# Kernel optimization log

Measured on AMD Instinct MI355X. Metric: run time of the kernel, lower is better.

Reference implementation:

```python
import jax, jax.numpy as jnp
import numpy as np

N = 200_000      # active voxels
C_IN = 128
C_OUT = 128
GRID = 128
K = 27           # 3x3x3 submanifold kernel offsets
EPS = 1e-4       # scn BatchNormalization default eps
LEAK = 0.333     # scn LeakyReLU default leakiness


def _build_neighbor_idx(rng):
    # unique active voxel coords via unique linear keys in GRID^3
    keys = rng.choice(GRID ** 3, size=N, replace=False).astype(np.int64)
    z = keys % GRID
    y = (keys // GRID) % GRID
    x = keys // (GRID * GRID)
    coords = np.stack([x, y, z], axis=1)  # [N,3]
    order = np.argsort(keys)
    sorted_keys = keys[order]
    offs = np.array([(dx, dy, dz) for dx in (-1, 0, 1)
                     for dy in (-1, 0, 1) for dz in (-1, 0, 1)], dtype=np.int64)
    nb = np.full((N, K), -1, dtype=np.int32)
    for k in range(K):
        q = coords + offs[k]  # [N,3]
        inb = np.all((q >= 0) & (q < GRID), axis=1)
        qk = (q[:, 0] * GRID + q[:, 1]) * GRID + q[:, 2]
        pos = np.searchsorted(sorted_keys, qk)
        pos = np.clip(pos, 0, N - 1)
        hit = inb & (sorted_keys[pos] == qk)
        nb[:, k] = np.where(hit, order[pos].astype(np.int32), -1)
    return nb


def setup_inputs() -> dict:
    key = jax.random.key(0)
    k1, k2 = jax.random.split(key)
    rng = np.random.default_rng(0)
    neighbor_idx = jnp.asarray(_build_neighbor_idx(rng))       # [N,27] int32, -1 = inactive
    features = jax.random.normal(k1, (N, C_IN), dtype=jnp.float32)
    # per-offset conv weights, scn-style init scale
    W = jax.random.normal(k2, (K, C_IN, C_OUT), dtype=jnp.float32) * (1.0 / np.sqrt(K * C_IN))
    b = jnp.zeros((C_OUT,), dtype=jnp.float32)
    gamma = jnp.ones((C_OUT,), dtype=jnp.float32)
    beta = jnp.zeros((C_OUT,), dtype=jnp.float32)
    return {"features": features, "W": W, "b": b, "gamma": gamma,
            "beta": beta, "neighbor_idx": neighbor_idx}


def reference(features, W, b, gamma, beta, neighbor_idx):
    # Submanifold 3D conv: output only at active sites; gather active neighbors.
    valid = (neighbor_idx >= 0)                      # [N,27] bool
    idx = jnp.where(valid, neighbor_idx, 0)          # safe gather index
    out = jnp.broadcast_to(b, (features.shape[0], C_OUT))
    for k in range(K):  # fixed structural loop over 27 kernel offsets
        xk = features[idx[:, k]] * valid[:, k:k + 1].astype(features.dtype)  # [N,C_IN]
        out = out + xk @ W[k]                                                # [N,C_OUT]
    # BatchNormalization over all active sites (training-mode batch stats)
    mean = jnp.mean(out, axis=0)
    var = jnp.var(out, axis=0)
    out = (out - mean) * jax.lax.rsqrt(var + EPS) * gamma + beta
    # LeakyReLU (scn default leakiness 0.333)
    return jnp.where(out > 0, out, LEAK * out)
```

## Files before the change

kernel.cpp:

```cpp
#include <hip/hip_runtime.h>
#include <hip/hip_bf16.h>

#define N_VOX 200000
#define CI 128
#define CO 128
#define KK 27
#define BM 128
#define NBLK 1563
#define NSTEP 54
#define LEAK 0.333f
#define BN_EPS 1e-4f

typedef unsigned short u16;
typedef unsigned int u32;
typedef __attribute__((ext_vector_type(8))) short short8;
typedef __attribute__((ext_vector_type(4))) float f32x4;

typedef const __attribute__((address_space(1))) u32* gptr_t;
typedef __attribute__((address_space(3))) u32* lptr_t;

__device__ __forceinline__ u16 f2bf(float f) {
  union { float f; u32 u; } x; x.f = f;
  return (u16)((x.u + 0x7FFFu + ((x.u >> 16) & 1u)) >> 16);
}
__device__ __forceinline__ u16 cvt_bf(float f) {
  union { __hip_bfloat16 h; u16 u; } c;
  c.h = __float2bfloat16(f);
  return c.u;
}

__global__ __launch_bounds__(256) void wcast_kernel(const float* __restrict__ W,
                                                    u16* __restrict__ Wt) {
  __shared__ float tile[32][33];
  int k = blockIdx.z;
  int ci0 = blockIdx.y * 32, co0 = blockIdx.x * 32;
  const float* Wk = W + (size_t)k * CI * CO;
  u16* Wtk = Wt + (size_t)k * CI * CO;
  int tx = threadIdx.x, ty = threadIdx.y;
#pragma unroll
  for (int j = 0; j < 4; ++j)
    tile[ty + j * 8][tx] = Wk[(ci0 + ty + j * 8) * CO + co0 + tx];
  __syncthreads();
#pragma unroll
  for (int j = 0; j < 4; ++j) {
    int co = co0 + ty + j * 8;
    int ci = ci0 + tx;
    Wtk[co * CI + (ci ^ ((co & 7) << 3))] = f2bf(tile[tx][ty + j * 8]);
  }
}

__global__ __launch_bounds__(256, 2) void conv_kernel(
    const float* __restrict__ feat, const u16* __restrict__ Wt,
    const int* __restrict__ nb, float* __restrict__ out,
    float* __restrict__ partial) {
  __shared__ __align__(16) char smem[79360];
  u16* const Ab0 = (u16*)smem;
  u16* const Ab1 = (u16*)(smem + 16384);
  u16* const Bb0 = (u16*)(smem + 32768);
  u16* const Bb1 = (u16*)(smem + 49152);
  int* const nbs = (int*)(smem + 65536);
  float* const sq = (float*)(smem + 65536);

  const int tid = threadIdx.x;
  const int bid = blockIdx.x;
  const int row0 = bid * BM;

  for (int i = tid; i < BM * KK; i += 256) {
    int gi = row0 * KK + i;
    nbs[i] = (gi < N_VOX * KK) ? nb[gi] : -1;
  }
  __syncthreads();

  const int lane = tid & 63;
  const int wv = tid >> 6;
  const int wr = wv >> 1, wc = wv & 1;
  const int lr = lane & 15, lg = lane >> 4;
  const int arow = tid >> 1;
  const int acol = (tid & 1) * 32;

  f32x4 acc[4][4];
#pragma unroll
  for (int m = 0; m < 4; ++m)
#pragma unroll
    for (int n = 0; n < 4; ++n) acc[m][n] = (f32x4){0.f, 0.f, 0.f, 0.f};

  float4 af[8];

  auto issueA = [&](int s) {
    int k = s >> 1, half = (s & 1) * 64;
    int src = nbs[arow * KK + k];
    if (src >= 0) {
      const float4* p = (const float4*)(feat + (size_t)src * CI + half + acol);
#pragma unroll
      for (int j = 0; j < 8; ++j) af[j] = p[j];
    } else {
#pragma unroll
      for (int j = 0; j < 8; ++j) af[j] = (float4){0.f, 0.f, 0.f, 0.f};
    }
  };

  auto issueB = [&](int s, u16* Bdst) {
    int k = s >> 1, half = (s & 1) * 64;
    const u16* base = Wt + (size_t)k * CO * CI + half;
#pragma unroll
    for (int j = 0; j < 4; ++j) {
      int cbase = (tid >> 6) * 64 + 256 * j;
      int c = cbase + (tid & 63);
      int co = c >> 3, sub = c & 7;
      gptr_t g = (gptr_t)(base + (size_t)co * CI + sub * 8);
      __builtin_amdgcn_global_load_lds(g, (lptr_t)(Bdst + cbase * 8), 16, 0, 0);
    }
  };

  auto writeA = [&](u16* Adst) {
    int v = arow & 7;
#pragma unroll
    for (int q = 0; q < 4; ++q) {
      u16 t8[8];
#pragma unroll
      for (int i = 0; i < 2; ++i) {
        float4 f = af[q * 2 + i];
        t8[i * 4 + 0] = cvt_bf(f.x); t8[i * 4 + 1] = cvt_bf(f.y);
        t8[i * 4 + 2] = cvt_bf(f.z); t8[i * 4 + 3] = cvt_bf(f.w);
      }
      int c_o = (tid & 1) * 4 + q;
      *(uint4*)&Adst[arow * 64 + ((c_o ^ v) << 3)] = *(const uint4*)t8;
    }
  };

  auto compute = [&](const u16* A, const u16* B) {
#pragma unroll
    for (int ks = 0; ks < 2; ++ks) {
      short8 a[4], b[4];
#pragma unroll
      for (int m = 0; m < 4; ++m) {
        int r = wr * 64 + m * 16 + lr;
        a[m] = *(const short8*)((const char*)(A + r * 64) +
                                ((ks * 64 + lg * 16) ^ ((r & 7) << 4)));
      }
#pragma unroll
      for (int n = 0; n < 4; ++n) {
        int cn = wc * 64 + n * 16 + lr;
        b[n] = *(const short8*)((const char*)(B + cn * 64) +
                                ((ks * 64 + lg * 16) ^ ((cn & 7) << 4)));
      }
#pragma unroll
      for (int m = 0; m < 4; ++m)
#pragma unroll
        for (int n = 0; n < 4; ++n)
          acc[m][n] = __builtin_amdgcn_mfma_f32_16x16x32_bf16(a[m], b[n], acc[m][n], 0, 0, 0);
    }
  };

  issueA(0);
  issueB(0, Bb0);
  for (int s = 0; s < NSTEP - 1; ++s) {
    int pb = s & 1;
    u16* Ac = pb ? Ab1 : Ab0;
    u16* Bc = pb ? Bb1 : Bb0;
    u16* Bn = pb ? Bb0 : Bb1;
    writeA(Ac);
    __syncthreads();
    issueA(s + 1);
    issueB(s + 1, Bn);
    compute(Ac, Bc);
  }
  writeA(Ab1);
  __syncthreads();
  compute(Ab1, Bb1);

  float sv[4], qv[4];
#pragma unroll
  for (int n = 0; n < 4; ++n) {
    float s = 0.f, q = 0.f;
    int col = wc * 64 + n * 16 + lr;
#pragma unroll
    for (int m = 0; m < 4; ++m) {
      int rb = row0 + wr * 64 + m * 16 + lg * 4;
#pragma unroll
      for (int e = 0; e < 4; ++e) {
        float x = acc[m][n][e];
        if (rb + e < N_VOX) out[(size_t)(rb + e) * CO + col] = x;
        s += x; q += x * x;
      }
    }
    s += __shfl_xor(s, 16, 64); s += __shfl_xor(s, 32, 64);
    q += __shfl_xor(q, 16, 64); q += __shfl_xor(q, 32, 64);
    sv[n] = s; qv[n] = q;
  }
  __syncthreads();
  if (lg == 0) {
#pragma unroll
    for (int n = 0; n < 4; ++n) {
      int col = wc * 64 + n * 16 + lr;
      sq[wr * 256 + col] = sv[n];
      sq[wr * 256 + 128 + col] = qv[n];
    }
  }
  __syncthreads();
  partial[(size_t)bid * 256 + tid] = sq[tid] + sq[256 + tid];
}

__global__ __launch_bounds__(256) void reduce1_kernel(const float* __restrict__ partial,
                                                      float* __restrict__ partial2) {
  int t = threadIdx.x, b = blockIdx.x;
  float acc = 0.f;
  int jend = (b + 1) * 16; if (jend > NBLK) jend = NBLK;
  for (int j = b * 16; j < jend; ++j) acc += partial[(size_t)j * 256 + t];
  partial2[(size_t)b * 256 + t] = acc;
}

__global__ __launch_bounds__(256) void reduce2_kernel(const float* __restrict__ partial2,
                                                      const float* __restrict__ gamma,
                                                      const float* __restrict__ beta,
                                                      float* __restrict__ stats) {
  __shared__ float sums[256];
  int t = threadIdx.x;
  float acc = 0.f;
  for (int j = 0; j < 98; ++j) acc += partial2[(size_t)j * 256 + t];
  sums[t] = acc;
  __syncthreads();
  if (t < 128) {
    float mean = sums[t] / (float)N_VOX;
    float var = sums[128 + t] / (float)N_VOX - mean * mean;
    float scale = gamma[t] * rsqrtf(var + BN_EPS);
    stats[t] = scale;
    stats[128 + t] = beta[t] - mean * scale;
  }
}

__global__ __launch_bounds__(256) void bnact_kernel(float* __restrict__ out,
                                                    const float* __restrict__ stats) {
  __shared__ float s_scale[128], s_shift[128];
  int t = threadIdx.x;
  if (t < 128) { s_scale[t] = stats[t]; s_shift[t] = stats[128 + t]; }
  __syncthreads();
  size_t i = (size_t)blockIdx.x * 256 + t;
  float4* o4 = (float4*)out;
  float4 v = o4[i];
  int c0 = ((int)(i & 31)) << 2;
  float x;
  x = v.x * s_scale[c0 + 0] + s_shift[c0 + 0]; v.x = x > 0.f ? x : LEAK * x;
  x = v.y * s_scale[c0 + 1] + s_shift[c0 + 1]; v.y = x > 0.f ? x : LEAK * x;
  x = v.z * s_scale[c0 + 2] + s_shift[c0 + 2]; v.z = x > 0.f ? x : LEAK * x;
  x = v.w * s_scale[c0 + 3] + s_shift[c0 + 3]; v.w = x > 0.f ? x : LEAK * x;
  o4[i] = v;
}

extern "C" void kernel_launch(void* const* d_in, const int* in_sizes, int n_in,
                              void* d_out, int out_size, void* d_ws, size_t ws_size,
                              hipStream_t stream) {
  const float* feat  = (const float*)d_in[0];
  const float* W     = (const float*)d_in[1];
  const float* gamma = (const float*)d_in[3];
  const float* beta  = (const float*)d_in[4];
  const int*   nb    = (const int*)d_in[5];
  float* out = (float*)d_out;

  char* ws = (char*)d_ws;
  u16*   Wt       = (u16*)ws;
  float* partial  = (float*)(ws + 884736);
  float* partial2 = (float*)(ws + 2485248);
  float* stats    = (float*)(ws + 2585600);

  hipLaunchKernelGGL(wcast_kernel, dim3(4, 4, 27), dim3(32, 8), 0, stream, W, Wt);
  hipLaunchKernelGGL(conv_kernel, dim3(NBLK), dim3(256), 0, stream, feat, Wt, nb, out, partial);
  hipLaunchKernelGGL(reduce1_kernel, dim3(98), dim3(256), 0, stream, partial, partial2);
  hipLaunchKernelGGL(reduce2_kernel, dim3(1), dim3(256), 0, stream, partial2, gamma, beta, stats);
  hipLaunchKernelGGL(bnact_kernel, dim3(25000), dim3(256), 0, stream, out, stats);
}
```

Baseline: 302.0 us.

## Pre-cast features to bf16 and gather A tiles directly into LDS

Adds a pass that converts the fp32 feature matrix to bf16 in workspace once. The conv kernel then gathers neighbor rows with global_load_lds straight into swizzled LDS, using a zeroed pad buffer for inactive neighbors. This removes the per-step register staging, bf16 conversion and LDS write of A, and halves gather bytes, at the cost of an extra full cast pass over the 100 MB input. It also raises wave priority around the MFMA section, and keeps the old kernel as a fallback when the workspace is too small.

```diff
diff --git a/kernel.cpp b/kernel.cpp
--- a/kernel.cpp
+++ b/kernel.cpp
@@ -29,6 +29,17 @@
   return c.u;
 }
 
+__global__ __launch_bounds__(256) void fcast_kernel(const float* __restrict__ f,
+                                                    u16* __restrict__ fb) {
+  size_t i = ((size_t)blockIdx.x * 256 + threadIdx.x) * 8;
+  float4 a = *(const float4*)(f + i);
+  float4 b = *(const float4*)(f + i + 4);
+  u16 t[8];
+  t[0] = cvt_bf(a.x); t[1] = cvt_bf(a.y); t[2] = cvt_bf(a.z); t[3] = cvt_bf(a.w);
+  t[4] = cvt_bf(b.x); t[5] = cvt_bf(b.y); t[6] = cvt_bf(b.z); t[7] = cvt_bf(b.w);
+  *(uint4*)(fb + i) = *(const uint4*)t;
+}
+
 __global__ __launch_bounds__(256) void wcast_kernel(const float* __restrict__ W,
                                                     u16* __restrict__ Wt) {
   __shared__ float tile[32][33];
@@ -50,6 +61,139 @@
 }
 
 __global__ __launch_bounds__(256, 2) void conv_kernel(
+    const u16* __restrict__ featb, const u16* __restrict__ Wt,
+    const int* __restrict__ nb, const u16* __restrict__ zp,
+    float* __restrict__ out, float* __restrict__ partial) {
+  __shared__ __align__(16) char smem[79360];
+  u16* const Ab0 = (u16*)smem;
+  u16* const Ab1 = (u16*)(smem + 16384);
+  u16* const Bb0 = (u16*)(smem + 32768);
+  u16* const Bb1 = (u16*)(smem + 49152);
+  int* const nbs = (int*)(smem + 65536);
+  float* const sq = (float*)smem;
+
+  const int tid = threadIdx.x;
+  const int bid = blockIdx.x;
+  const int row0 = bid * BM;
+
+  for (int i = tid; i < BM * KK; i += 256) {
+    int gi = row0 * KK + i;
+    nbs[i] = (gi < N_VOX * KK) ? nb[gi] : -1;
+  }
+  __syncthreads();
+
+  const int lane = tid & 63;
+  const int wv = tid >> 6;
+  const int wr = wv >> 1, wc = wv & 1;
+  const int lr = lane & 15, lg = lane >> 4;
+
+  f32x4 acc[4][4];
+#pragma unroll
+  for (int m = 0; m < 4; ++m)
+#pragma unroll
+    for (int n = 0; n < 4; ++n) acc[m][n] = (f32x4){0.f, 0.f, 0.f, 0.f};
+
+  auto issueA = [&](int s, u16* Adst) {
+    int k = s >> 1;
+    int halfU = (s & 1) * 64;
+    int r = tid >> 3;
+    int cl = tid & 7;
+#pragma unroll
+    for (int j = 0; j < 4; ++j) {
+      int row = j * 32 + r;
+      int src = nbs[row * KK + k];
+      const u16* g = (src >= 0) ? (featb + (size_t)src * CI + halfU) : zp;
+      g += ((cl ^ (row & 7)) << 3);
+      __builtin_amdgcn_global_load_lds((gptr_t)g, (lptr_t)(Adst + (j * 32 + wv * 8) * 64),
+                                       16, 0, 0);
+    }
+  };
+
+  auto issueB = [&](int s, u16* Bdst) {
+    int k = s >> 1;
+    int halfU = (s & 1) * 64;
+    const u16* base = Wt + (size_t)k * CI * CO + halfU;
+#pragma unroll
+    for (int j = 0; j < 4; ++j) {
+      int cb = (j * 4 + wv) * 64;
+      int c = cb + lane;
+      int co = c >> 3, sub = c & 7;
+      __builtin_amdgcn_global_load_lds((gptr_t)(base + co * CI + sub * 8),
+                                       (lptr_t)(Bdst + cb * 8), 16, 0, 0);
+    }
+  };
+
+  auto compute = [&](const u16* A, const u16* B) {
+    __builtin_amdgcn_s_setprio(1);
+#pragma unroll
+    for (int ks = 0; ks < 2; ++ks) {
+      short8 a[4], b[4];
+#pragma unroll
+      for (int m = 0; m < 4; ++m) {
+        int r = wr * 64 + m * 16 + lr;
+        a[m] = *(const short8*)((const char*)(A + r * 64) +
+                                ((ks * 64 + lg * 16) ^ ((r & 7) << 4)));
+      }
+#pragma unroll
+      for (int n = 0; n < 4; ++n) {
+        int cn = wc * 64 + n * 16 + lr;
+        b[n] = *(const short8*)((const char*)(B + cn * 64) +
+                                ((ks * 64 + lg * 16) ^ ((cn & 7) << 4)));
+      }
+#pragma unroll
+      for (int m = 0; m < 4; ++m)
+#pragma unroll
+        for (int n = 0; n < 4; ++n)
+          acc[m][n] = __builtin_amdgcn_mfma_f32_16x16x32_bf16(a[m], b[n], acc[m][n], 0, 0, 0);
+    }
+    __builtin_amdgcn_s_setprio(0);
+  };
+
+  issueA(0, Ab0);
+  issueB(0, Bb0);
+  for (int s = 0; s < NSTEP; ++s) {
+    __syncthreads();
+    int pb = s & 1;
+    if (s + 1 < NSTEP) {
+      issueA(s + 1, pb ? Ab0 : Ab1);
+      issueB(s + 1, pb ? Bb0 : Bb1);
+    }
+    compute(pb ? Ab1 : Ab0, pb ? Bb1 : Bb0);
+  }
+
+  float sv[4], qv[4];
+#pragma unroll
+  for (int n = 0; n < 4; ++n) {
+    float s = 0.f, q = 0.f;
+    int col = wc * 64 + n * 16 + lr;
+#pragma unroll
+    for (int m = 0; m < 4; ++m) {
+      int rb = row0 + wr * 64 + m * 16 + lg * 4;
+#pragma unroll
+      for (int e = 0; e < 4; ++e) {
+        float x = acc[m][n][e];
+        if (rb + e < N_VOX) out[(size_t)(rb + e) * CO + col] = x;
+        s += x; q += x * x;
+      }
+    }
+    s += __shfl_xor(s, 16, 64); s += __shfl_xor(s, 32, 64);
+    q += __shfl_xor(q, 16, 64); q += __shfl_xor(q, 32, 64);
+    sv[n] = s; qv[n] = q;
+  }
+  __syncthreads();
+  if (lg == 0) {
+#pragma unroll
+    for (int n = 0; n < 4; ++n) {
+      int col = wc * 64 + n * 16 + lr;
+      sq[wr * 256 + col] = sv[n];
+      sq[wr * 256 + 128 + col] = qv[n];
+    }
+  }
+  __syncthreads();
+  partial[(size_t)bid * 256 + tid] = sq[tid] + sq[256 + tid];
+}
+
+__global__ __launch_bounds__(256, 2) void conv_fb_kernel(
     const float* __restrict__ feat, const u16* __restrict__ Wt,
     const int* __restrict__ nb, float* __restrict__ out,
     float* __restrict__ partial) {
@@ -59,7 +203,7 @@
   u16* const Bb0 = (u16*)(smem + 32768);
   u16* const Bb1 = (u16*)(smem + 49152);
   int* const nbs = (int*)(smem + 65536);
-  float* const sq = (float*)(smem + 65536);
+  float* const sq = (float*)smem;
 
   const int tid = threadIdx.x;
   const int bid = blockIdx.x;
@@ -85,7 +229,6 @@
     for (int n = 0; n < 4; ++n) acc[m][n] = (f32x4){0.f, 0.f, 0.f, 0.f};
 
   float4 af[8];
-
   auto issueA = [&](int s) {
     int k = s >> 1, half = (s & 1) * 64;
     int src = nbs[arow * KK + k];
@@ -98,20 +241,18 @@
       for (int j = 0; j < 8; ++j) af[j] = (float4){0.f, 0.f, 0.f, 0.f};
     }
   };
-
   auto issueB = [&](int s, u16* Bdst) {
     int k = s >> 1, half = (s & 1) * 64;
     const u16* base = Wt + (size_t)k * CO * CI + half;
 #pragma unroll
     for (int j = 0; j < 4; ++j) {
-      int cbase = (tid >> 6) * 64 + 256 * j;
-      int c = cbase + (tid & 63);
+      int cb = (j * 4 + wv) * 64;
+      int c = cb + lane;
       int co = c >> 3, sub = c & 7;
-      gptr_t g = (gptr_t)(base + (size_t)co * CI + sub * 8);
-      __builtin_amdgcn_global_load_lds(g, (lptr_t)(Bdst + cbase * 8), 16, 0, 0);
-    }
-  };
-
+      __builtin_amdgcn_global_load_lds((gptr_t)(base + co * CI + sub * 8),
+                                       (lptr_t)(Bdst + cb * 8), 16, 0, 0);
+    }
+  };
   auto writeA = [&](u16* Adst) {
     int v = arow & 7;
 #pragma unroll
@@ -127,7 +268,6 @@
       *(uint4*)&Adst[arow * 64 + ((c_o ^ v) << 3)] = *(const uint4*)t8;
     }
   };
-
   auto compute = [&](const u16* A, const u16* B) {
 #pragma unroll
     for (int ks = 0; ks < 2; ++ks) {
@@ -262,9 +402,20 @@
   float* partial  = (float*)(ws + 884736);
   float* partial2 = (float*)(ws + 2485248);
   float* stats    = (float*)(ws + 2585600);
+  u16*   zp       = (u16*)(ws + 2586624);
+  u16*   featb    = (u16*)(ws + 2586880);
+  const size_t need_fast = 2586880u + 51200000u;
 
   hipLaunchKernelGGL(wcast_kernel, dim3(4, 4, 27), dim3(32, 8), 0, stream, W, Wt);
-  hipLaunchKernelGGL(conv_kernel, dim3(NBLK), dim3(256), 0, stream, feat, Wt, nb, out, partial);
+  if (ws_size >= need_fast) {
+    hipMemsetAsync(zp, 0, 256, stream);
+    hipLaunchKernelGGL(fcast_kernel, dim3(12500), dim3(256), 0, stream, feat, featb);
+    hipLaunchKernelGGL(conv_kernel, dim3(NBLK), dim3(256), 0, stream,
+                       featb, Wt, nb, zp, out, partial);
+  } else {
+    hipLaunchKernelGGL(conv_fb_kernel, dim3(NBLK), dim3(256), 0, stream,
+                       feat, Wt, nb, out, partial);
+  }
   hipLaunchKernelGGL(reduce1_kernel, dim3(98), dim3(256), 0, stream, partial, partial2);
   hipLaunchKernelGGL(reduce2_kernel, dim3(1), dim3(256), 0, stream, partial2, gamma, beta, stats);
   hipLaunchKernelGGL(bnact_kernel, dim3(25000), dim3(256), 0, stream, out, stats);
```

Result: faster. 288.9 us (-4.4%).
